# Performance work log

Measured on AMD Instinct MI355X. Metric: run time of the kernel, lower is better.

Reference implementation:

```python
import jax, jax.numpy as jnp
import numpy as np

TOLX = 1e-12
TOLFUN = 1e-06
MAXITER = 1000
ALPHA = 1e-4
MIN_LAMBDA = 0.1
MAX_LAMBDA = 0.5
MAX_STEPS = 10  # fixed unroll budget; Newton converges in < 10 iterations for this problem
BS, NY = 200000, 8


def setup_inputs():
    key = jax.random.key(0)
    k1, k2, k3 = jax.random.split(key, 3)
    y0 = jax.random.normal(k1, (BS, NY), dtype=jnp.float32)
    W = 0.1 * jax.random.normal(k2, (NY, NY), dtype=jnp.float32)
    V = 0.1 * jax.random.normal(k3, (NY, NY), dtype=jnp.float32)
    dt = jnp.asarray(0.1, dtype=jnp.float32)
    t = jnp.asarray(1.0, dtype=jnp.float32)
    return {"y0": y0, "dt": dt, "t": t, "W": W, "V": V}


def _safe_div(n, d, eps=1e-30):
    ok = jnp.abs(d) > eps
    return jnp.where(ok, n / jnp.where(ok, d, 1.0), 0.0)


def _solver(y0, dt, t, W, V):
    bs, ny = y0.shape
    one = jnp.float32(1.0)

    def delta_S(tt, y):
        # test ODE right-hand side g(t, y): mildly nonlinear, acts per-sample
        return jnp.tanh(y @ W) @ V - 0.1 * y + 0.01 * jnp.sin(tt)

    def err(y):  # implicit-Euler residual, (bs, ny)
        return (y - y0) / dt - delta_S(t, y)

    def _err_single(yb, y0b):
        return (yb - y0b) / dt - (jnp.tanh(yb @ W) @ V - 0.1 * yb + 0.01 * jnp.sin(t))

    def batched_jac(y):
        # (bs, ny, ny): d err_b / d y_b; matches torch batch-diagonal of autograd jacobian
        return jax.vmap(jax.jacfwd(_err_single), in_axes=(0, 0))(y, y0)

    F0 = err(y0)
    jac0 = batched_jac(y0)
    rn0 = jnp.max(jnp.abs(F0), axis=1)
    fobj0 = jnp.einsum('bi,bi->b', F0, F0)

    state0 = dict(y=y0, yold=y0, F=F0, dy=jnp.zeros_like(y0), jac=jac0,
                  resnorm=rn0, resnorm0=100.0 * rn0,
                  lam=one, lam1=one, lam2=jnp.float32(0.5),
                  fold=fobj0, f2=fobj0, slope=jnp.zeros((bs,), y0.dtype),
                  lam_min=jnp.float32(0.0), niter=jnp.int32(0), exitflag=jnp.int32(1))

    def body(s, _):
        active = (((jnp.max(s['resnorm']) > TOLFUN) | (s['lam'] < 1.0))
                  & (s['exitflag'] >= 0) & (s['niter'] <= MAXITER))

        # --- lam == 1: fresh Newton direction, slope, objective ---
        is_newton = s['lam'] == 1.0
        recompute = jnp.max(_safe_div(s['resnorm'], s['resnorm0'])) > 0.2
        fresh_jac = batched_jac(s['y'])
        jac = jnp.where(is_newton & recompute, fresh_jac, s['jac'])
        dy_n = -jnp.linalg.solve(jac, s['F'][..., None])[..., 0]  # lstsq on square == solve
        gvec = jnp.einsum('bi,bij->bj', s['F'], jac)
        slope_n = jnp.einsum('bj,bj->b', gvec, dy_n)
        fold_n = jnp.einsum('bi,bi->b', s['F'], s['F'])
        lam_min_n = _safe_div(jnp.float32(TOLX),
                              jnp.max(jnp.abs(dy_n) / jnp.maximum(jnp.abs(s['y']), 1.0)))

        dy = jnp.where(is_newton, dy_n, s['dy'])
        slope = jnp.where(is_newton, slope_n, s['slope'])
        fold = jnp.where(is_newton, fold_n, s['fold'])
        yold = jnp.where(is_newton, s['y'], s['yold'])
        lam_min = jnp.where(is_newton, lam_min_n, s['lam_min'])
        niter = jnp.where(is_newton, s['niter'] + 1, s['niter'])

        brk = s['lam'] < lam_min            # -> exitflag = 2, freeze state
        bad = ~jnp.all(jnp.isfinite(dy))    # -> exitflag = -1, freeze state

        # --- trial step + trust-region line search ---
        lam = s['lam']
        y_new = yold + dy * lam
        F_new = err(y_new)
        f_obj = jnp.einsum('bi,bi->b', F_new, F_new)
        lam1 = lam
        lam2, f2 = s['lam2'], s['f2']

        backtrack = jnp.any(f_obj > fold + ALPHA * lam * slope)
        # quadratic model (first backtrack)
        lam_quad = jnp.min(_safe_div(-slope / 2.0, f_obj - fold - slope))
        # cubic model (subsequent backtracks)
        A = _safe_div(one, lam1 - lam2)
        inv1 = _safe_div(one, lam1 * lam1)
        inv2 = _safe_div(one, lam2 * lam2)
        B = jnp.stack([jnp.stack([inv1, -inv2]), jnp.stack([-lam2 * inv1, lam1 * inv2])])
        C = jnp.stack([f_obj - fold - lam1 * slope, f2 - fold - lam2 * slope])  # (2, bs)
        ab = A * (B @ C)
        a, b = ab[0], ab[1]
        disc = b * b - 3.0 * a * slope
        sq = jnp.sqrt(jnp.maximum(disc, 0.0))
        lam_tmp = jnp.where(jnp.all(a == 0.0), _safe_div(-slope, 2.0 * b),
                   jnp.where(jnp.any(disc < 0.0), MAX_LAMBDA * lam1,
                    jnp.where(jnp.any(b <= 0.0), _safe_div(-b + sq, 3.0 * a),
                     _safe_div(-slope, b + sq))))
        lam_cubic = jnp.min(jnp.minimum(lam_tmp, MAX_LAMBDA * lam1))
        lam_bt = jnp.where(lam == 1.0, lam_quad, lam_cubic)
        nanf = ~jnp.all(jnp.isfinite(f_obj))
        lam_new = jnp.where(backtrack, lam_bt, jnp.where(nanf, MAX_LAMBDA * lam1, one))

        cont = lam_new < 1.0  # retry with smaller lambda next iteration (the `continue` path)
        lam2_new = jnp.where(cont, lam1, lam2)
        f2_new = jnp.where(cont, f_obj, f2)
        lam_new = jnp.where(cont, jnp.maximum(lam_new, MIN_LAMBDA * lam1), lam_new)
        resnorm_new = jnp.where(cont, s['resnorm'], jnp.max(jnp.abs(F_new), axis=1))
        resnorm0_new = jnp.where(cont, s['resnorm0'], s['resnorm'])

        upd = active & (~brk) & (~bad)
        exitflag = jnp.where(active & brk, jnp.int32(2),
                    jnp.where(active & (~brk) & bad, jnp.int32(-1), s['exitflag']))
        sel = lambda new, old: jnp.where(upd, new, old)

        ns = dict(y=sel(y_new, s['y']), yold=sel(yold, s['yold']), F=sel(F_new, s['F']),
                  dy=sel(dy, s['dy']), jac=sel(jac, s['jac']),
                  resnorm=sel(resnorm_new, s['resnorm']), resnorm0=sel(resnorm0_new, s['resnorm0']),
                  lam=sel(lam_new, s['lam']), lam1=sel(lam1, s['lam1']), lam2=sel(lam2_new, s['lam2']),
                  fold=sel(fold, s['fold']), f2=sel(f2_new, s['f2']), slope=sel(slope, s['slope']),
                  lam_min=sel(lam_min, s['lam_min']),
                  niter=jnp.where(active, niter, s['niter']), exitflag=exitflag)
        return ns, None

    sN, _ = jax.lax.scan(body, state0, None, length=MAX_STEPS)
    return sN['y'], sN['F'], sN['exitflag']


def reference(y0, dt, t, W, V):
    y, F, exitflag = _solver(y0, dt, t, W, V)
    return (y, F, exitflag)
```

## Files before the change

### kernel.cpp

```cpp
#include <hip/hip_runtime.h>
#include <hip/hip_cooperative_groups.h>

namespace cg = cooperative_groups;

#define BSZ 200000
#define NSTEPS 10
#define TOLFUN_C 1e-6f
#define ALPHA_C 1e-4f

#define CNTHR 256
#define CNBLK 256
#define CNT   (CNBLK*CNTHR)
#define SPT   4

#define FNTHR 256
#define FNBLK ((BSZ + FNTHR - 1)/FNTHR)

#define OFF_Y     ((size_t)0)
#define OFF_YOLD  ((size_t)BSZ*8)
#define OFF_DY    ((size_t)BSZ*16)
#define OFF_SJ    ((size_t)BSZ*24)
#define OFF_FOLD  ((size_t)BSZ*32)
#define OFF_SLOPE ((size_t)BSZ*33)
#define OFF_RESN  ((size_t)BSZ*34)
#define OFF_F2    ((size_t)BSZ*35)
#define OFF_TFO   ((size_t)BSZ*36)
#define OFF_TRN   ((size_t)BSZ*37)
#define OFF_R     ((size_t)BSZ*38)

#define RSTRIDE 64
#define NSLOT   9
#define R_TOT   (2 + NSTEPS*NSLOT)
#define KEY_MAX_IDENT 0x007FFFFFu
#define KEY_MIN_IDENT 0xFF800000u

static __device__ __forceinline__ float nanmax2(float a, float b){
    return (__builtin_isnan(a) || __builtin_isnan(b)) ? __builtin_nanf("") : fmaxf(a, b);
}
static __device__ __forceinline__ float nanmin2(float a, float b){
    return (__builtin_isnan(a) || __builtin_isnan(b)) ? __builtin_nanf("") : fminf(a, b);
}
static __device__ __forceinline__ float safe_div(float n, float d){
    return (fabsf(d) > 1e-30f) ? (n / d) : 0.0f;
}
static __device__ __forceinline__ unsigned fkey(float x){
    unsigned u = __float_as_uint(x);
    return (u & 0x80000000u) ? ~u : (u | 0x80000000u);
}
static __device__ __forceinline__ float funkey(unsigned u){
    return (u & 0x80000000u) ? __uint_as_float(u & 0x7FFFFFFFu) : __uint_as_float(~u);
}
static __device__ __forceinline__ unsigned fkey_max(float x){
    if (__builtin_isnan(x)) x = __uint_as_float(0x7FC00000u);
    return fkey(x);
}
static __device__ __forceinline__ unsigned fkey_min(float x){
    if (__builtin_isnan(x)) x = __uint_as_float(0xFFC00000u);
    return fkey(x);
}
static __device__ __forceinline__ void ld8(const float* p, float* v){
    float4 a = ((const float4*)p)[0], b = ((const float4*)p)[1];
    v[0]=a.x; v[1]=a.y; v[2]=a.z; v[3]=a.w; v[4]=b.x; v[5]=b.y; v[6]=b.z; v[7]=b.w;
}
static __device__ __forceinline__ void st8(float* p, const float* v){
    float4 a, b;
    a.x=v[0]; a.y=v[1]; a.z=v[2]; a.w=v[3];
    b.x=v[4]; b.y=v[5]; b.z=v[6]; b.w=v[7];
    ((float4*)p)[0]=a; ((float4*)p)[1]=b;
}
static __device__ __forceinline__ unsigned ldslot(const unsigned* p){
    return __hip_atomic_load(p, __ATOMIC_RELAXED, __HIP_MEMORY_SCOPE_AGENT);
}
static __device__ __forceinline__ void stslot(unsigned* p, unsigned v){
    __hip_atomic_store(p, v, __ATOMIC_RELAXED, __HIP_MEMORY_SCOPE_AGENT);
}

static __device__ __forceinline__ void computeFz(
    const float* yv, const float* y0v, float dt, float c0,
    const float* sW, const float* sV, float* Fo, float* zo)
{
    float u[8];
    #pragma unroll
    for (int k=0;k<8;k++){
        float acc = 0.f;
        #pragma unroll
        for (int m=0;m<8;m++) acc += yv[m]*sW[m*8+k];
        u[k]=acc;
    }
    #pragma unroll
    for (int k=0;k<8;k++) zo[k] = tanhf(u[k]);
    #pragma unroll
    for (int i=0;i<8;i++){
        float tv = 0.f;
        #pragma unroll
        for (int k=0;k<8;k++) tv += zo[k]*sV[k*8+i];
        Fo[i] = (yv[i]-y0v[i])/dt - ((tv - 0.1f*yv[i]) + c0);
    }
}

static __device__ __forceinline__ void devInit2(const float* y0v,
    float* yold, float* dy, float* sj,
    float& fold_o, float& slope_o, float& resn_o, float& f2_o,
    float dt, float c0, const float* sW, const float* sV,
    float& rn_red, float& rat_red)
{
    #pragma unroll
    for (int i=0;i<8;i++){ yold[i]=y0v[i]; dy[i]=0.f; }
    float Fv[8], z[8];
    computeFz(y0v, y0v, dt, c0, sW, sV, Fv, z);
    #pragma unroll
    for (int k=0;k<8;k++) sj[k] = 1.0f - z[k]*z[k];
    float fold = 0.f;
    #pragma unroll
    for (int i=0;i<8;i++) fold += Fv[i]*Fv[i];
    float rn0 = fabsf(Fv[0]);
    #pragma unroll
    for (int i=1;i<8;i++) rn0 = nanmax2(rn0, fabsf(Fv[i]));
    fold_o=fold; slope_o=0.f; resn_o=rn0; f2_o=fold;
    rn_red  = nanmax2(rn_red, rn0);
    rat_red = nanmax2(rat_red, safe_div(rn0, 100.0f*rn0));
}

static __device__ __forceinline__ void devA2(const float* y_cur, const float* y0v,
    float* yold, float* dy, float* sj, float& fold_o, float& slope_o,
    float dt, float invdt, float c0, const float* sW, const float* sV,
    bool recompute, float& gml, bool& nf)
{
    float Fv[8], z[8];
    computeFz(y_cur, y0v, dt, c0, sW, sV, Fv, z);
    if (recompute){
        #pragma unroll
        for (int k=0;k<8;k++) sj[k] = 1.0f - z[k]*z[k];
    }
    float J[8][8];
    #pragma unroll
    for (int j=0;j<8;j++){
        float zj[8];
        #pragma unroll
        for (int k=0;k<8;k++) zj[k] = sW[j*8+k]*sj[k];
        #pragma unroll
        for (int i=0;i<8;i++){
            float acc = 0.f;
            #pragma unroll
            for (int k=0;k<8;k++) acc += zj[k]*sV[k*8+i];
            J[i][j] = (i==j) ? (invdt - (acc - 0.1f)) : (0.0f - acc);
        }
    }
    float fold = 0.f;
    #pragma unroll
    for (int i=0;i<8;i++) fold += Fv[i]*Fv[i];
    float gv[8];
    #pragma unroll
    for (int j=0;j<8;j++){
        float acc = 0.f;
        #pragma unroll
        for (int i=0;i<8;i++) acc += Fv[i]*J[i][j];
        gv[j]=acc;
    }
    float x[8];
    #pragma unroll
    for (int i=0;i<8;i++) x[i]=Fv[i];
    #pragma unroll
    for (int c=0;c<8;c++){
        float ip = 1.0f / J[c][c];
        #pragma unroll
        for (int r2=c+1;r2<8;r2++){
            float m = J[r2][c]*ip;
            #pragma unroll
            for (int jj=c+1;jj<8;jj++) J[r2][jj] -= m*J[c][jj];
            x[r2] -= m*x[c];
        }
    }
    float wv[8];
    #pragma unroll
    for (int c=7;c>=0;c--){
        float acc = x[c];
        #pragma unroll
        for (int jj=c+1;jj<8;jj++) acc -= J[c][jj]*wv[jj];
        wv[c] = acc / J[c][c];
    }
    #pragma unroll
    for (int i=0;i<8;i++){
        yold[i] = y_cur[i];
        dy[i]   = -wv[i];
    }
    float slope = 0.f;
    #pragma unroll
    for (int j=0;j<8;j++) slope += gv[j]*dy[j];
    fold_o = fold; slope_o = slope;
    #pragma unroll
    for (int i=0;i<8;i++){
        float rr = fabsf(dy[i]) / nanmax2(fabsf(y_cur[i]), 1.0f);
        gml = nanmax2(gml, rr);
        nf = nf || !__builtin_isfinite(dy[i]);
    }
}

static __device__ __forceinline__ void devB2(const float* yold, const float* dy,
    const float* y0v, float foldv, float slopev, float resnv, float f2v,
    float dt, float c0, const float* sW, const float* sV, float lam, float lam2v,
    float& tfo_o, float& trn_o,
    bool& armijo, float& lq, bool& aNot0, bool& dN, bool& ble,
    float& mX, float& mZ, float& mW, bool& nanf, float& trnR, float& ratR)
{
    float yn[8];
    #pragma unroll
    for (int i=0;i<8;i++) yn[i] = yold[i] + dy[i]*lam;
    float Ft[8], z[8];
    computeFz(yn, y0v, dt, c0, sW, sV, Ft, z);
    float f_obj = 0.f;
    #pragma unroll
    for (int i=0;i<8;i++) f_obj += Ft[i]*Ft[i];
    float rn = fabsf(Ft[0]);
    #pragma unroll
    for (int i=1;i<8;i++) rn = nanmax2(rn, fabsf(Ft[i]));
    tfo_o = f_obj; trn_o = rn;
    armijo = armijo || (f_obj > (foldv + (ALPHA_C*lam)*slopev));
    lq = nanmin2(lq, safe_div((-slopev)*0.5f, (f_obj - foldv) - slopev));
    float lam1v = lam;
    float Af = safe_div(1.0f, lam1v - lam2v);
    float i1 = safe_div(1.0f, lam1v*lam1v);
    float i2 = safe_div(1.0f, lam2v*lam2v);
    float Cc0 = (f_obj - foldv) - lam1v*slopev;
    float Cc1 = (f2v   - foldv) - lam2v*slopev;
    float av = Af*(i1*Cc0 - i2*Cc1);
    float bv = Af*((-(lam2v*i1))*Cc0 + (lam1v*i2)*Cc1);
    float disc = bv*bv - (3.0f*av)*slopev;
    float dm = __builtin_isnan(disc) ? disc : fmaxf(disc, 0.0f);
    float sq = sqrtf(dm);
    aNot0 = aNot0 || (av != 0.0f);
    dN    = dN    || (disc < 0.0f);
    ble   = ble   || (bv <= 0.0f);
    mX = nanmin2(mX, safe_div(-slopev, 2.0f*bv));
    mZ = nanmin2(mZ, safe_div(-bv + sq, 3.0f*av));
    mW = nanmin2(mW, safe_div(-slopev, bv + sq));
    nanf = nanf || !__builtin_isfinite(f_obj);
    trnR = nanmax2(trnR, rn);
    ratR = nanmax2(ratR, safe_div(rn, resnv));
}

struct ScalarState {
    float lam, lam1, lam2, lam_min, maxrn, ratmax;
    int   niter, exitflag;
    bool  upd_prev, cont_prev;
};

static __device__ void advance(ScalarState& s, const unsigned* R, int j){
    const unsigned* r = R + (size_t)(2 + j*NSLOT)*RSTRIDE;
    unsigned v0 = ldslot(r + (size_t)0*RSTRIDE);
    unsigned v1 = ldslot(r + (size_t)1*RSTRIDE);
    unsigned v2 = ldslot(r + (size_t)2*RSTRIDE);
    unsigned v3 = ldslot(r + (size_t)3*RSTRIDE);
    unsigned v4 = ldslot(r + (size_t)4*RSTRIDE);
    unsigned v5 = ldslot(r + (size_t)5*RSTRIDE);
    unsigned v6 = ldslot(r + (size_t)6*RSTRIDE);
    unsigned v7 = ldslot(r + (size_t)7*RSTRIDE);
    unsigned v8 = ldslot(r + (size_t)8*RSTRIDE);
    bool active    = ((s.maxrn > TOLFUN_C) || (s.lam < 1.0f)) && (s.exitflag >= 0) && (s.niter <= 1000);
    bool is_newton = (s.lam == 1.0f);
    float lam_min_new = is_newton ? safe_div(1e-12f, funkey(v0)) : s.lam_min;
    bool brk = (s.lam < lam_min_new);
    bool bad = is_newton ? (v1 != 0u) : false;
    bool upd = active && !brk && !bad;
    int niter_new = active ? (is_newton ? s.niter + 1 : s.niter) : s.niter;
    int ef_new = s.exitflag;
    if (active && brk) ef_new = 2;
    else if (active && !brk && bad) ef_new = -1;
    bool cont = false;
    if (upd){
        float lam1c = s.lam;
        unsigned bm = v8;
        bool backtrack = (bm & 1u) != 0u;
        float lamq  = funkey(v2);
        bool allA0  = (bm & 2u) == 0u;
        bool anyDN  = (bm & 4u) != 0u;
        bool anyB0  = (bm & 8u) != 0u;
        float lam_tmp_min = allA0 ? funkey(v3)
                          : (anyDN ? (0.5f*lam1c)
                          : (anyB0 ? funkey(v4) : funkey(v5)));
        float lam_cubic = nanmin2(lam_tmp_min, 0.5f*lam1c);
        float lam_bt = (s.lam == 1.0f) ? lamq : lam_cubic;
        bool nanf = (bm & 16u) != 0u;
        float lam_new = backtrack ? lam_bt : (nanf ? 0.5f*lam1c : 1.0f);
        cont = (lam_new < 1.0f);
        float lam2_new = cont ? lam1c : s.lam2;
        if (cont) lam_new = nanmax2(lam_new, 0.1f*lam1c);
        float maxrn_new  = cont ? s.maxrn  : funkey(v6);
        float ratmax_new = cont ? s.ratmax : funkey(v7);
        s.lam = lam_new; s.lam1 = lam1c; s.lam2 = lam2_new;
        s.lam_min = lam_min_new; s.maxrn = maxrn_new; s.ratmax = ratmax_new;
    }
    s.niter = niter_new; s.exitflag = ef_new;
    s.upd_prev = upd; s.cont_prev = cont;
}

static __device__ ScalarState replayN(const unsigned* R, int n){
    ScalarState s;
    s.lam=1.0f; s.lam1=1.0f; s.lam2=0.5f; s.lam_min=0.0f;
    s.maxrn  = funkey(ldslot(&R[0]));
    s.ratmax = funkey(ldslot(&R[(size_t)1*RSTRIDE]));
    s.niter=0; s.exitflag=1; s.upd_prev=false; s.cont_prev=false;
    for (int j=0;j<n;++j) advance(s, R, j);
    return s;
}

__global__ __launch_bounds__(CNTHR, 1) void kFused(
    const float* __restrict__ y0g, const float* __restrict__ Wm, const float* __restrict__ Vm,
    const float* __restrict__ dtp, const float* __restrict__ tp,
    float* __restrict__ ws, float* __restrict__ out)
{
    cg::grid_group gridg = cg::this_grid();
    __shared__ float sW[64], sV[64];
    __shared__ float redF[6][4];
    __shared__ unsigned redB[4];
    int t = threadIdx.x;
    if (t < 64) sW[t] = Wm[t];
    else if (t < 128) sV[t-64] = Vm[t-64];
    unsigned* R = (unsigned*)(ws + OFF_R);
    if (blockIdx.x == 0 && t < R_TOT){
        unsigned v;
        if (t < 2) v = KEY_MAX_IDENT;
        else {
            int off = (t - 2) % NSLOT;
            bool ismin = (off==2 || off==3 || off==4 || off==5);
            bool ismax = (off==0 || off==6 || off==7);
            v = ismin ? KEY_MIN_IDENT : (ismax ? KEY_MAX_IDENT : 0u);
        }
        stslot(&R[(size_t)t*RSTRIDE], v);
    }
    __syncthreads();
    gridg.sync();

    int gtid = blockIdx.x*CNTHR + t;
    float dt = *dtp, invdt = 1.0f/dt, c0 = 0.01f*sinf(*tp);

    bool  valid[SPT];
    float y0r[SPT][8], yold[SPT][8], dyv[SPT][8], sjv[SPT][8];
    float foldv[SPT], slopev[SPT], resnv[SPT], f2v[SPT], tfov[SPT], trnv[SPT];
    float lamc = 0.0f;

    float rn_red = -__builtin_inff(), rat_red = -__builtin_inff();
    #pragma unroll
    for (int q=0;q<SPT;q++){
        int sid = gtid + q*CNT;
        valid[q] = sid < BSZ;
        if (valid[q]){
            ld8(y0g + (size_t)sid*8, y0r[q]);
            devInit2(y0r[q], yold[q], dyv[q], sjv[q],
                     foldv[q], slopev[q], resnv[q], f2v[q],
                     dt, c0, sW, sV, rn_red, rat_red);
            tfov[q]=0.f; trnv[q]=0.f;
        } else {
            #pragma unroll
            for (int i=0;i<8;i++){ y0r[q][i]=0; yold[q][i]=0; dyv[q][i]=0; sjv[q][i]=0; }
            foldv[q]=0; slopev[q]=0; resnv[q]=0; f2v[q]=0; tfov[q]=0; trnv[q]=0;
        }
    }
    #pragma unroll
    for (int o=32;o>=1;o>>=1){
        rn_red  = nanmax2(rn_red,  __shfl_xor(rn_red,  o, 64));
        rat_red = nanmax2(rat_red, __shfl_xor(rat_red, o, 64));
    }
    {
        int w = t >> 6;
        if ((t & 63) == 0){ redF[0][w] = rn_red; redF[1][w] = rat_red; }
        __syncthreads();
        if (t == 0){
            float a = redF[0][0];
            #pragma unroll
            for (int w2=1;w2<4;w2++) a = nanmax2(a, redF[0][w2]);
            atomicMax(&R[0], fkey_max(a));
        } else if (t == 1){
            float b = redF[1][0];
            #pragma unroll
            for (int w2=1;w2<4;w2++) b = nanmax2(b, redF[1][w2]);
            atomicMax(&R[(size_t)1*RSTRIDE], fkey_max(b));
        }
    }
    gridg.sync();

    ScalarState S;
    S.lam=1.0f; S.lam1=1.0f; S.lam2=0.5f; S.lam_min=0.0f;
    S.maxrn  = funkey(ldslot(&R[0]));
    S.ratmax = funkey(ldslot(&R[(size_t)1*RSTRIDE]));
    S.niter=0; S.exitflag=1; S.upd_prev=false; S.cont_prev=false;

    #pragma unroll 1
    for (int k=1; k<=NSTEPS; ++k){
        if (S.upd_prev){
            lamc = S.lam1;
            #pragma unroll
            for (int q=0;q<SPT;q++){
                if (!valid[q]) continue;
                if (S.cont_prev) f2v[q]  = tfov[q];
                else             resnv[q] = trnv[q];
            }
        }
        bool active    = ((S.maxrn > TOLFUN_C) || (S.lam < 1.0f)) && (S.exitflag >= 0) && (S.niter <= 1000);
        bool is_newton = (S.lam == 1.0f);
        unsigned* r = R + (size_t)(2 + (k-1)*NSLOT)*RSTRIDE;

        if (active && is_newton){
            bool recompute = (S.ratmax > 0.2f);
            float gml = -__builtin_inff(); bool nf = false;
            #pragma unroll
            for (int q=0;q<SPT;q++){
                if (!valid[q]) continue;
                float y_cur[8];
                #pragma unroll
                for (int i=0;i<8;i++) y_cur[i] = yold[q][i] + dyv[q][i]*lamc;
                devA2(y_cur, y0r[q], yold[q], dyv[q], sjv[q], foldv[q], slopev[q],
                      dt, invdt, c0, sW, sV, recompute, gml, nf);
            }
            lamc = 0.0f;
            #pragma unroll
            for (int o=32;o>=1;o>>=1) gml = nanmax2(gml, __shfl_xor(gml, o, 64));
            unsigned long long anym = __ballot(nf ? 1 : 0);
            int w = t >> 6;
            if ((t & 63) == 0){ redF[0][w] = gml; redB[w] = anym ? 1u : 0u; }
            __syncthreads();
            if (t == 0){
                float v = redF[0][0];
                #pragma unroll
                for (int w2=1;w2<4;w2++) v = nanmax2(v, redF[0][w2]);
                atomicMax(&r[0], fkey_max(v));
            } else if (t == 1){
                unsigned bm = redB[0]|redB[1]|redB[2]|redB[3];
                if (bm) atomicOr(&r[(size_t)1*RSTRIDE], 1u);
            }
            __syncthreads();
        }

        if (active){
            float lam = S.lam, lam2v = S.lam2;
            bool armijo=false, aNot0=false, dN=false, ble=false, nanf=false;
            float lq=__builtin_inff(), mX=__builtin_inff(), mZ=__builtin_inff(), mW=__builtin_inff();
            float trnR=-__builtin_inff(), ratR=-__builtin_inff();
            #pragma unroll
            for (int q=0;q<SPT;q++){
                if (!valid[q]) continue;
                devB2(yold[q], dyv[q], y0r[q], foldv[q], slopev[q], resnv[q], f2v[q],
                      dt, c0, sW, sV, lam, lam2v, tfov[q], trnv[q],
                      armijo, lq, aNot0, dN, ble, mX, mZ, mW, nanf, trnR, ratR);
            }
            #pragma unroll
            for (int o=32;o>=1;o>>=1){
                lq   = nanmin2(lq,   __shfl_xor(lq,   o, 64));
                mX   = nanmin2(mX,   __shfl_xor(mX,   o, 64));
                mZ   = nanmin2(mZ,   __shfl_xor(mZ,   o, 64));
                mW   = nanmin2(mW,   __shfl_xor(mW,   o, 64));
                trnR = nanmax2(trnR, __shfl_xor(trnR, o, 64));
                ratR = nanmax2(ratR, __shfl_xor(ratR, o, 64));
            }
            unsigned long long bArm = __ballot(armijo ? 1 : 0);
            unsigned long long bA0  = __ballot(aNot0  ? 1 : 0);
            unsigned long long bDN  = __ballot(dN     ? 1 : 0);
            unsigned long long bB0  = __ballot(ble    ? 1 : 0);
            unsigned long long bNF  = __ballot(nanf   ? 1 : 0);
            int w = t >> 6;
            if ((t & 63) == 0){
                redF[0][w]=lq; redF[1][w]=mX; redF[2][w]=mZ; redF[3][w]=mW;
                redF[4][w]=trnR; redF[5][w]=ratR;
                redB[w] = (bArm?1u:0u) | (bA0?2u:0u) | (bDN?4u:0u) | (bB0?8u:0u) | (bNF?16u:0u);
            }
            __syncthreads();
            if (t < 6){
                float v = redF[t][0];
                bool ismin = (t < 4);
                #pragma unroll
                for (int w2=1;w2<4;w2++) v = ismin ? nanmin2(v, redF[t][w2]) : nanmax2(v, redF[t][w2]);
                unsigned* p = &r[(size_t)(t + 2)*RSTRIDE];
                if (ismin) atomicMin(p, fkey_min(v));
                else       atomicMax(p, fkey_max(v));
            } else if (t == 6){
                unsigned bm = redB[0]|redB[1]|redB[2]|redB[3];
                if (bm) atomicOr(&r[(size_t)8*RSTRIDE], bm);
            }
        }

        gridg.sync();
        advance(S, R, k-1);
    }

    if (S.upd_prev) lamc = S.lam1;
    #pragma unroll
    for (int q=0;q<SPT;q++){
        if (!valid[q]) continue;
        int sid = gtid + q*CNT;
        float yf[8];
        #pragma unroll
        for (int i=0;i<8;i++) yf[i] = yold[q][i] + dyv[q][i]*lamc;
        st8(out + (size_t)sid*8, yf);
        float Fv[8], z[8];
        computeFz(yf, y0r[q], dt, c0, sW, sV, Fv, z);
        st8(out + (size_t)BSZ*8 + (size_t)sid*8, Fv);
    }
    if (gtid == 0) out[(size_t)BSZ*16] = (float)S.exitflag;
}

__global__ void kPre(unsigned* __restrict__ R){
    int i = threadIdx.x;
    if (i >= R_TOT) return;
    unsigned v;
    if (i < 2) v = KEY_MAX_IDENT;
    else {
        int off = (i - 2) % NSLOT;
        bool ismin = (off==2 || off==3 || off==4 || off==5);
        bool ismax = (off==0 || off==6 || off==7);
        v = ismin ? KEY_MIN_IDENT : (ismax ? KEY_MAX_IDENT : 0u);
    }
    R[(size_t)i*RSTRIDE] = v;
}

__global__ __launch_bounds__(FNTHR) void fInit(
    const float* __restrict__ y0g, const float* __restrict__ Wm, const float* __restrict__ Vm,
    const float* __restrict__ dtp, const float* __restrict__ tp, float* __restrict__ ws)
{
    __shared__ float sW[64], sV[64];
    __shared__ float red[2][4];
    int t = threadIdx.x;
    if (t < 64) sW[t] = Wm[t];
    else if (t < 128) sV[t-64] = Vm[t-64];
    __syncthreads();
    unsigned* R = (unsigned*)(ws + OFF_R);
    int tid = blockIdx.x*FNTHR + t;
    bool valid = tid < BSZ;
    float dt = *dtp, c0 = 0.01f*sinf(*tp);
    float rn_red = -__builtin_inff(), rat_red = -__builtin_inff();
    if (valid){
        float y0v[8], yo[8], dv[8], sj[8], fold, slope, resn, f2;
        ld8(y0g + (size_t)tid*8, y0v);
        devInit2(y0v, yo, dv, sj, fold, slope, resn, f2, dt, c0, sW, sV, rn_red, rat_red);
        st8(ws+OFF_Y   +(size_t)tid*8, y0v);
        st8(ws+OFF_YOLD+(size_t)tid*8, yo);
        st8(ws+OFF_DY  +(size_t)tid*8, dv);
        st8(ws+OFF_SJ  +(size_t)tid*8, sj);
        ws[OFF_FOLD+tid]=fold; ws[OFF_SLOPE+tid]=slope;
        ws[OFF_RESN+tid]=resn; ws[OFF_F2+tid]=f2;
        ws[OFF_TFO+tid]=0.f;   ws[OFF_TRN+tid]=0.f;
    }
    #pragma unroll
    for (int o=32;o>=1;o>>=1){
        rn_red  = nanmax2(rn_red,  __shfl_xor(rn_red,  o, 64));
        rat_red = nanmax2(rat_red, __shfl_xor(rat_red, o, 64));
    }
    int w = t >> 6;
    if ((t & 63) == 0){ red[0][w]=rn_red; red[1][w]=rat_red; }
    __syncthreads();
    if (t == 0){
        float a = red[0][0];
        for (int w2=1;w2<4;w2++) a = nanmax2(a, red[0][w2]);
        atomicMax(&R[0], fkey_max(a));
    } else if (t == 1){
        float b = red[1][0];
        for (int w2=1;w2<4;w2++) b = nanmax2(b, red[1][w2]);
        atomicMax(&R[(size_t)1*RSTRIDE], fkey_max(b));
    }
}

__global__ __launch_bounds__(FNTHR) void fStep(
    const float* __restrict__ y0g, const float* __restrict__ Wm, const float* __restrict__ Vm,
    const float* __restrict__ dtp, const float* __restrict__ tp,
    float* __restrict__ ws, int step)
{
    __shared__ float sW[64], sV[64];
    __shared__ float redF[6][4];
    __shared__ unsigned redB[4];
    int t = threadIdx.x;
    if (t < 64) sW[t] = Wm[t];
    else if (t < 128) sV[t-64] = Vm[t-64];
    __syncthreads();
    unsigned* R = (unsigned*)(ws + OFF_R);
    ScalarState S = replayN(R, step-1);
    bool active    = ((S.maxrn > TOLFUN_C) || (S.lam < 1.0f)) && (S.exitflag >= 0) && (S.niter <= 1000);
    bool is_newton = (S.lam == 1.0f);
    if (!S.upd_prev && !active) return;

    int tid = blockIdx.x*FNTHR + t;
    bool valid = tid < BSZ;
    float dt = *dtp, invdt = 1.0f/dt, c0 = 0.01f*sinf(*tp);
    unsigned* r = R + (size_t)(2 + (step-1)*NSLOT)*RSTRIDE;

    float y0v[8], yv[8], yo[8], dv[8], sj[8], fold=0, slope=0, resn=0, f2=0;
    if (valid){
        ld8(y0g + (size_t)tid*8, y0v);
        ld8(ws+OFF_Y   +(size_t)tid*8, yv);
        ld8(ws+OFF_YOLD+(size_t)tid*8, yo);
        ld8(ws+OFF_DY  +(size_t)tid*8, dv);
        ld8(ws+OFF_SJ  +(size_t)tid*8, sj);
        fold=ws[OFF_FOLD+tid]; slope=ws[OFF_SLOPE+tid];
        resn=ws[OFF_RESN+tid]; f2=ws[OFF_F2+tid];
        if (S.upd_prev){
            #pragma unroll
            for (int i=0;i<8;i++) yv[i] = yo[i] + dv[i]*S.lam1;
            st8(ws+OFF_Y+(size_t)tid*8, yv);
            if (S.cont_prev){ f2 = ws[OFF_TFO+tid];  ws[OFF_F2+tid]   = f2; }
            else            { resn = ws[OFF_TRN+tid]; ws[OFF_RESN+tid] = resn; }
        }
    }
    if (!active) return;

    if (is_newton){
        bool recompute = (S.ratmax > 0.2f);
        float gml = -__builtin_inff(); bool nf = false;
        if (valid){
            devA2(yv, y0v, yo, dv, sj, fold, slope, dt, invdt, c0, sW, sV, recompute, gml, nf);
            st8(ws+OFF_YOLD+(size_t)tid*8, yo);
            st8(ws+OFF_DY  +(size_t)tid*8, dv);
            if (recompute) st8(ws+OFF_SJ+(size_t)tid*8, sj);
            ws[OFF_FOLD+tid]  = fold;
            ws[OFF_SLOPE+tid] = slope;
        }
        #pragma unroll
        for (int o=32;o>=1;o>>=1) gml = nanmax2(gml, __shfl_xor(gml, o, 64));
        unsigned long long anym = __ballot(nf ? 1 : 0);
        int w = t >> 6;
        if ((t & 63) == 0){ redF[0][w] = gml; redB[w] = anym ? 1u : 0u; }
        __syncthreads();
        if (t == 0){
            float v = redF[0][0];
            for (int w2=1;w2<4;w2++) v = nanmax2(v, redF[0][w2]);
            atomicMax(&r[0], fkey_max(v));
        } else if (t == 1){
            unsigned bm = redB[0]|redB[1]|redB[2]|redB[3];
            if (bm) atomicOr(&r[(size_t)1*RSTRIDE], 1u);
        }
        __syncthreads();
    }

    {
        float lam = S.lam, lam2v = S.lam2;
        bool armijo=false, aNot0=false, dN=false, ble=false, nanf=false;
        float lq=__builtin_inff(), mX=__builtin_inff(), mZ=__builtin_inff(), mW=__builtin_inff();
        float trnR=-__builtin_inff(), ratR=-__builtin_inff();
        if (valid){
            float tfo, trn;
            devB2(yo, dv, y0v, fold, slope, resn, f2, dt, c0, sW, sV, lam, lam2v,
                  tfo, trn, armijo, lq, aNot0, dN, ble, mX, mZ, mW, nanf, trnR, ratR);
            ws[OFF_TFO+tid] = tfo;
            ws[OFF_TRN+tid] = trn;
        }
        #pragma unroll
        for (int o=32;o>=1;o>>=1){
            lq   = nanmin2(lq,   __shfl_xor(lq,   o, 64));
            mX   = nanmin2(mX,   __shfl_xor(mX,   o, 64));
            mZ   = nanmin2(mZ,   __shfl_xor(mZ,   o, 64));
            mW   = nanmin2(mW,   __shfl_xor(mW,   o, 64));
            trnR = nanmax2(trnR, __shfl_xor(trnR, o, 64));
            ratR = nanmax2(ratR, __shfl_xor(ratR, o, 64));
        }
        unsigned long long bArm = __ballot(armijo ? 1 : 0);
        unsigned long long bA0  = __ballot(aNot0  ? 1 : 0);
        unsigned long long bDN  = __ballot(dN     ? 1 : 0);
        unsigned long long bB0  = __ballot(ble    ? 1 : 0);
        unsigned long long bNF  = __ballot(nanf   ? 1 : 0);
        int w = t >> 6;
        if ((t & 63) == 0){
            redF[0][w]=lq; redF[1][w]=mX; redF[2][w]=mZ; redF[3][w]=mW;
            redF[4][w]=trnR; redF[5][w]=ratR;
            redB[w] = (bArm?1u:0u) | (bA0?2u:0u) | (bDN?4u:0u) | (bB0?8u:0u) | (bNF?16u:0u);
        }
        __syncthreads();
        if (t < 6){
            float v = redF[t][0];
            bool ismin = (t < 4);
            for (int w2=1;w2<4;w2++) v = ismin ? nanmin2(v, redF[t][w2]) : nanmax2(v, redF[t][w2]);
            unsigned* p = &r[(size_t)(t + 2)*RSTRIDE];
            if (ismin) atomicMin(p, fkey_min(v));
            else       atomicMax(p, fkey_max(v));
        } else if (t == 6){
            unsigned bm = redB[0]|redB[1]|redB[2]|redB[3];
            if (bm) atomicOr(&r[(size_t)8*RSTRIDE], bm);
        }
    }
}

__global__ __launch_bounds__(FNTHR) void fOut(
    const float* __restrict__ y0g, const float* __restrict__ Wm, const float* __restrict__ Vm,
    const float* __restrict__ dtp, const float* __restrict__ tp,
    const float* __restrict__ ws, float* __restrict__ out)
{
    __shared__ float sW[64], sV[64];
    int t = threadIdx.x;
    if (t < 64) sW[t] = Wm[t];
    else if (t < 128) sV[t-64] = Vm[t-64];
    __syncthreads();
    const unsigned* R = (const unsigned*)(ws + OFF_R);
    ScalarState S = replayN(R, NSTEPS);
    int tid = blockIdx.x*FNTHR + t;
    float dt = *dtp, c0 = 0.01f*sinf(*tp);
    if (tid < BSZ){
        float y0v[8], yv[8];
        ld8(y0g + (size_t)tid*8, y0v);
        ld8(ws+OFF_Y+(size_t)tid*8, yv);
        if (S.upd_prev){
            float yo[8], dv[8];
            ld8(ws+OFF_YOLD+(size_t)tid*8, yo);
            ld8(ws+OFF_DY  +(size_t)tid*8, dv);
            #pragma unroll
            for (int i=0;i<8;i++) yv[i] = yo[i] + dv[i]*S.lam1;
        }
        st8(out + (size_t)tid*8, yv);
        float Fv[8], z[8];
        computeFz(yv, y0v, dt, c0, sW, sV, Fv, z);
        st8(out + (size_t)BSZ*8 + (size_t)tid*8, Fv);
    }
    if (blockIdx.x == 0 && t == 0) out[(size_t)BSZ*16] = (float)S.exitflag;
}

extern "C" void kernel_launch(void* const* d_in, const int* in_sizes, int n_in,
                              void* d_out, int out_size, void* d_ws, size_t ws_size,
                              hipStream_t stream)
{
    const float* y0g = (const float*)d_in[0];
    const float* dtp = (const float*)d_in[1];
    const float* tp  = (const float*)d_in[2];
    const float* Wm  = (const float*)d_in[3];
    const float* Vm  = (const float*)d_in[4];
    float* ws   = (float*)d_ws;
    float* outp = (float*)d_out;

    void* args[] = {(void*)&y0g, (void*)&Wm, (void*)&Vm, (void*)&dtp, (void*)&tp,
                    (void*)&ws, (void*)&outp};
    hipError_t rc = hipLaunchCooperativeKernel((const void*)kFused, dim3(CNBLK), dim3(CNTHR),
                                               args, 0, stream);
    if (rc != hipSuccess){
        hipLaunchKernelGGL(kPre, dim3(1), dim3(128), 0, stream, (unsigned*)(ws + OFF_R));
        hipLaunchKernelGGL(fInit, dim3(FNBLK), dim3(FNTHR), 0, stream, y0g, Wm, Vm, dtp, tp, ws);
        for (int s = 1; s <= NSTEPS; ++s)
            hipLaunchKernelGGL(fStep, dim3(FNBLK), dim3(FNTHR), 0, stream, y0g, Wm, Vm, dtp, tp, ws, s);
        hipLaunchKernelGGL(fOut, dim3(FNBLK), dim3(FNTHR), 0, stream, y0g, Wm, Vm, dtp, tp, ws, outp);
    }
}
```

Baseline: 524.9 us.

## Double block size, halve samples per thread, move y0 into shared memory

Block size grows from 256 to 512 threads and samples per thread drop from 4 to 2, so the same 256 cooperative blocks cover the batch with twice as many resident waves. The per-sample y0 vectors are moved from registers into a shared-memory array read back at each use, lowering register pressure so the larger block fits. Block reductions are widened to 8 waves. The trade is extra LDS traffic and 32KB of shared memory per block in exchange for more latency hiding.

```diff
diff --git a/kernel.cpp b/kernel.cpp
--- a/kernel.cpp
+++ b/kernel.cpp
@@ -8,10 +8,11 @@
 #define TOLFUN_C 1e-6f
 #define ALPHA_C 1e-4f
 
-#define CNTHR 256
+#define CNTHR 512
 #define CNBLK 256
 #define CNT   (CNBLK*CNTHR)
-#define SPT   4
+#define SPT   2
+#define SLOTS (CNTHR*SPT)
 
 #define FNTHR 256
 #define FNBLK ((BSZ + FNTHR - 1)/FNTHR)
@@ -311,8 +312,9 @@
 {
     cg::grid_group gridg = cg::this_grid();
     __shared__ float sW[64], sV[64];
-    __shared__ float redF[6][4];
-    __shared__ unsigned redB[4];
+    __shared__ float sY0[8*SLOTS];
+    __shared__ float redF[6][8];
+    __shared__ unsigned redB[8];
     int t = threadIdx.x;
     if (t < 64) sW[t] = Wm[t];
     else if (t < 128) sV[t-64] = Vm[t-64];
@@ -335,7 +337,7 @@
     float dt = *dtp, invdt = 1.0f/dt, c0 = 0.01f*sinf(*tp);
 
     bool  valid[SPT];
-    float y0r[SPT][8], yold[SPT][8], dyv[SPT][8], sjv[SPT][8];
+    float yold[SPT][8], dyv[SPT][8], sjv[SPT][8];
     float foldv[SPT], slopev[SPT], resnv[SPT], f2v[SPT], tfov[SPT], trnv[SPT];
     float lamc = 0.0f;
 
@@ -343,16 +345,20 @@
     #pragma unroll
     for (int q=0;q<SPT;q++){
         int sid = gtid + q*CNT;
+        int slot = q*CNTHR + t;
         valid[q] = sid < BSZ;
         if (valid[q]){
-            ld8(y0g + (size_t)sid*8, y0r[q]);
-            devInit2(y0r[q], yold[q], dyv[q], sjv[q],
+            float y0v[8];
+            ld8(y0g + (size_t)sid*8, y0v);
+            #pragma unroll
+            for (int i=0;i<8;i++) sY0[i*SLOTS + slot] = y0v[i];
+            devInit2(y0v, yold[q], dyv[q], sjv[q],
                      foldv[q], slopev[q], resnv[q], f2v[q],
                      dt, c0, sW, sV, rn_red, rat_red);
             tfov[q]=0.f; trnv[q]=0.f;
         } else {
             #pragma unroll
-            for (int i=0;i<8;i++){ y0r[q][i]=0; yold[q][i]=0; dyv[q][i]=0; sjv[q][i]=0; }
+            for (int i=0;i<8;i++){ sY0[i*SLOTS + slot]=0; yold[q][i]=0; dyv[q][i]=0; sjv[q][i]=0; }
             foldv[q]=0; slopev[q]=0; resnv[q]=0; f2v[q]=0; tfov[q]=0; trnv[q]=0;
         }
     }
@@ -368,12 +374,12 @@
         if (t == 0){
             float a = redF[0][0];
             #pragma unroll
-            for (int w2=1;w2<4;w2++) a = nanmax2(a, redF[0][w2]);
+            for (int w2=1;w2<8;w2++) a = nanmax2(a, redF[0][w2]);
             atomicMax(&R[0], fkey_max(a));
         } else if (t == 1){
             float b = redF[1][0];
             #pragma unroll
-            for (int w2=1;w2<4;w2++) b = nanmax2(b, redF[1][w2]);
+            for (int w2=1;w2<8;w2++) b = nanmax2(b, redF[1][w2]);
             atomicMax(&R[(size_t)1*RSTRIDE], fkey_max(b));
         }
     }
@@ -406,10 +412,14 @@
             #pragma unroll
             for (int q=0;q<SPT;q++){
                 if (!valid[q]) continue;
-                float y_cur[8];
+                int slot = q*CNTHR + t;
+                float y_cur[8], y0v[8];
                 #pragma unroll
-                for (int i=0;i<8;i++) y_cur[i] = yold[q][i] + dyv[q][i]*lamc;
-                devA2(y_cur, y0r[q], yold[q], dyv[q], sjv[q], foldv[q], slopev[q],
+                for (int i=0;i<8;i++){
+                    y_cur[i] = yold[q][i] + dyv[q][i]*lamc;
+                    y0v[i]   = sY0[i*SLOTS + slot];
+                }
+                devA2(y_cur, y0v, yold[q], dyv[q], sjv[q], foldv[q], slopev[q],
                       dt, invdt, c0, sW, sV, recompute, gml, nf);
             }
             lamc = 0.0f;
@@ -422,10 +432,12 @@
             if (t == 0){
                 float v = redF[0][0];
                 #pragma unroll
-                for (int w2=1;w2<4;w2++) v = nanmax2(v, redF[0][w2]);
+                for (int w2=1;w2<8;w2++) v = nanmax2(v, redF[0][w2]);
                 atomicMax(&r[0], fkey_max(v));
             } else if (t == 1){
-                unsigned bm = redB[0]|redB[1]|redB[2]|redB[3];
+                unsigned bm = 0u;
+                #pragma unroll
+                for (int w2=0;w2<8;w2++) bm |= redB[w2];
                 if (bm) atomicOr(&r[(size_t)1*RSTRIDE], 1u);
             }
             __syncthreads();
@@ -439,7 +451,11 @@
             #pragma unroll
             for (int q=0;q<SPT;q++){
                 if (!valid[q]) continue;
-                devB2(yold[q], dyv[q], y0r[q], foldv[q], slopev[q], resnv[q], f2v[q],
+                int slot = q*CNTHR + t;
+                float y0v[8];
+                #pragma unroll
+                for (int i=0;i<8;i++) y0v[i] = sY0[i*SLOTS + slot];
+                devB2(yold[q], dyv[q], y0v, foldv[q], slopev[q], resnv[q], f2v[q],
                       dt, c0, sW, sV, lam, lam2v, tfov[q], trnv[q],
                       armijo, lq, aNot0, dN, ble, mX, mZ, mW, nanf, trnR, ratR);
             }
@@ -468,12 +484,14 @@
                 float v = redF[t][0];
                 bool ismin = (t < 4);
                 #pragma unroll
-                for (int w2=1;w2<4;w2++) v = ismin ? nanmin2(v, redF[t][w2]) : nanmax2(v, redF[t][w2]);
+                for (int w2=1;w2<8;w2++) v = ismin ? nanmin2(v, redF[t][w2]) : nanmax2(v, redF[t][w2]);
                 unsigned* p = &r[(size_t)(t + 2)*RSTRIDE];
                 if (ismin) atomicMin(p, fkey_min(v));
                 else       atomicMax(p, fkey_max(v));
             } else if (t == 6){
-                unsigned bm = redB[0]|redB[1]|redB[2]|redB[3];
+                unsigned bm = 0u;
+                #pragma unroll
+                for (int w2=0;w2<8;w2++) bm |= redB[w2];
                 if (bm) atomicOr(&r[(size_t)8*RSTRIDE], bm);
             }
         }
@@ -487,12 +505,16 @@
     for (int q=0;q<SPT;q++){
         if (!valid[q]) continue;
         int sid = gtid + q*CNT;
-        float yf[8];
-        #pragma unroll
-        for (int i=0;i<8;i++) yf[i] = yold[q][i] + dyv[q][i]*lamc;
+        int slot = q*CNTHR + t;
+        float yf[8], y0v[8];
+        #pragma unroll
+        for (int i=0;i<8;i++){
+            yf[i]  = yold[q][i] + dyv[q][i]*lamc;
+            y0v[i] = sY0[i*SLOTS + slot];
+        }
         st8(out + (size_t)sid*8, yf);
         float Fv[8], z[8];
-        computeFz(yf, y0r[q], dt, c0, sW, sV, Fv, z);
+        computeFz(yf, y0v, dt, c0, sW, sV, Fv, z);
         st8(out + (size_t)BSZ*8 + (size_t)sid*8, Fv);
     }
     if (gtid == 0) out[(size_t)BSZ*16] = (float)S.exitflag;
```

Result: slower. 580.3 us (+10.5%).
